# Kernel optimization log

Hardware: AMD Instinct MI355X
Metric: run time of the kernel (lower is better)

## Reference

```python
import jax, jax.numpy as jnp
import numpy as np

STACK_DEPTH = 16
SHARPEN = 5.0
LN_EPS = 1e-5
EPS = 1e-8


def _apply_tools(x, tw):
    # tools: relu, gelu(exact), tanh, sigmoid, identity; tw: [B, 5]
    return (jax.nn.relu(x) * tw[:, 0:1]
            + jax.nn.gelu(x, approximate=False) * tw[:, 1:2]
            + jnp.tanh(x) * tw[:, 2:3]
            + jax.nn.sigmoid(x) * tw[:, 3:4]
            + x * tw[:, 4:5])


def _forward(hidden_states, W_proj, b_proj, W_op, b_op, W_tool, b_tool, ln_gamma, ln_beta):
    B, S, H = hidden_states.shape
    D = STACK_DEPTH

    # Per-timestep linear ops are time-independent -> batch them up front.
    proj = jnp.einsum('bsh,ph->bsp', hidden_states, W_proj) + b_proj  # [B,S,2H]
    h_all, v_all = proj[..., :H], proj[..., H:]
    op_probs = jax.nn.softmax(jnp.einsum('bsh,oh->bso', hidden_states, W_op) + b_op, axis=-1)  # [B,S,3]
    tool_w = jax.nn.softmax(jnp.einsum('bsh,th->bst', h_all, W_tool) + b_tool, axis=-1)  # [B,S,T]

    # Differentiable stack recurrence (push/pop/nop with pointer sharpening).
    stack0 = jnp.zeros((B, D, H), hidden_states.dtype)
    pointer0 = jnp.zeros((B, D), hidden_states.dtype).at[:, 0].set(1.0)

    def step(carry, xs):
        stack, pointer = carry
        value, ops = xs  # value: [B,H], ops: [B,3]
        push, pop, nop = ops[:, 0:1], ops[:, 1:2], ops[:, 2:3]
        p_push = jnp.roll(pointer, 1, axis=1)   # pointer moves up on push
        p_pop = jnp.roll(pointer, -1, axis=1)   # pointer moves down on pop
        new_p = push * p_push + pop * p_pop + nop * pointer
        new_p = new_p ** SHARPEN
        new_p = new_p / (jnp.sum(new_p, axis=1, keepdims=True) + EPS)
        w = (push * p_push)[..., None]          # [B,D,1] write weight at pushed slot
        new_stack = stack * (1.0 - w) + value[:, None, :] * w
        top = jnp.sum(new_stack * new_p[..., None], axis=1)  # [B,H]
        return (new_stack, new_p), top

    (stack_f, pointer_f), tops = jax.lax.scan(
        step, (stack0, pointer0),
        (jnp.swapaxes(v_all, 0, 1), jnp.swapaxes(op_probs, 0, 1)))
    tops = jnp.swapaxes(tops, 0, 1)  # [B,S,H]

    processed = jax.vmap(_apply_tools, in_axes=(1, 1), out_axes=1)(tops, tool_w)  # [B,S,H]
    combined = h_all + processed + hidden_states

    mu = jnp.mean(combined, axis=-1, keepdims=True)
    var = jnp.mean((combined - mu) ** 2, axis=-1, keepdims=True)
    final = (combined - mu) * jax.lax.rsqrt(var + LN_EPS) * ln_gamma + ln_beta
    return final, stack_f, pointer_f, tool_w


def setup_inputs() -> dict:
    key = jax.random.key(0)
    ks = jax.random.split(key, 4)
    B, S, H, T = 16, 2048, 1024, 5
    sd = 1.0 / np.sqrt(H)
    return {
        'hidden_states': jax.random.normal(ks[0], (B, S, H), jnp.float32),
        'W_proj': jax.random.normal(ks[1], (2 * H, H), jnp.float32) * sd,
        'b_proj': jnp.zeros((2 * H,), jnp.float32),
        'W_op': jax.random.normal(ks[2], (3, H), jnp.float32) * sd,
        'b_op': jnp.zeros((3,), jnp.float32),
        'W_tool': jax.random.normal(ks[3], (T, H), jnp.float32) * sd,
        'b_tool': jnp.zeros((T,), jnp.float32),
        'ln_gamma': jnp.ones((H,), jnp.float32),
        'ln_beta': jnp.zeros((H,), jnp.float32),
    }


def reference(hidden_states, W_proj, b_proj, W_op, b_op, W_tool, b_tool, ln_gamma, ln_beta):
    return _forward(hidden_states, W_proj, b_proj, W_op, b_op, W_tool, b_tool, ln_gamma, ln_beta)
```

## Files before the change

kernel.cpp:

```cpp
#include <hip/hip_runtime.h>
#include <hip/hip_bf16.h>
#include <cstdint>
#include <cstdio>


typedef float f32x4 __attribute__((ext_vector_type(4)));
typedef __bf16 bf8v __attribute__((ext_vector_type(8)));

#define WS_ABF   0ULL
#define WS_WBF   67108864ULL
#define WS_PROJ  71303168ULL
#define WS_OP4   205520896ULL
#define WS_WP    206045184ULL
#define WS_NEED  210239488ULL

#define OUT_FINAL 0
#define OUT_STACK 33554432ULL
#define OUT_PTR   33816576ULL
#define OUT_TOOLW 33816832ULL
#define SLE_OFF   0ULL
#define ATOT_OFF  30000000ULL

__device__ __forceinline__ float bf2f(unsigned short u) {
    union { unsigned int i; float f; } v; v.i = ((unsigned int)u) << 16; return v.f;
}
__device__ __forceinline__ unsigned short f2bf(float f) {
    __hip_bfloat16 h = __float2bfloat16(f);
    return __builtin_bit_cast(unsigned short, h);
}
template<int C>
__device__ __forceinline__ float fdpp(float x) {
    return __int_as_float(__builtin_amdgcn_mov_dpp(__float_as_int(x), C, 0xF, 0xF, true));
}
__device__ __forceinline__ void gload_lds16(const void* g, void* l) {
    __builtin_amdgcn_global_load_lds(
        (__attribute__((address_space(1))) void*)(uintptr_t)g,
        (__attribute__((address_space(3))) void*)l,
        16, 0, 0);
}

__global__ __launch_bounds__(256) void k0(const float* __restrict__ hid,
                                          const float* __restrict__ Wp,
                                          const float* __restrict__ Wop,
                                          const float* __restrict__ bop,
                                          unsigned short* __restrict__ Abf,
                                          unsigned short* __restrict__ Wbf,
                                          float4* __restrict__ op4)
{
    const int bid = blockIdx.x, tid = threadIdx.x;
    if (bid < 8192) {
        const int wid = tid >> 6, lane = tid & 63;
        const int row = bid * 4 + wid;
        const float* hrow = hid + (size_t)row * 1024 + lane * 16;
        float xs[16];
        #pragma unroll
        for (int j = 0; j < 4; ++j) {
            float4 t = *(const float4*)(hrow + j * 4);
            xs[j*4+0] = t.x; xs[j*4+1] = t.y; xs[j*4+2] = t.z; xs[j*4+3] = t.w;
        }
        unsigned short us[16];
        #pragma unroll
        for (int j = 0; j < 16; ++j) us[j] = f2bf(xs[j]);
        uint4 ulo, uhi;
        ulo.x = (unsigned)us[0]  | ((unsigned)us[1]  << 16);
        ulo.y = (unsigned)us[2]  | ((unsigned)us[3]  << 16);
        ulo.z = (unsigned)us[4]  | ((unsigned)us[5]  << 16);
        ulo.w = (unsigned)us[6]  | ((unsigned)us[7]  << 16);
        uhi.x = (unsigned)us[8]  | ((unsigned)us[9]  << 16);
        uhi.y = (unsigned)us[10] | ((unsigned)us[11] << 16);
        uhi.z = (unsigned)us[12] | ((unsigned)us[13] << 16);
        uhi.w = (unsigned)us[14] | ((unsigned)us[15] << 16);
        unsigned short* arow = Abf + (size_t)row * 1024 + lane * 16;
        *(uint4*)(arow)     = ulo;
        *(uint4*)(arow + 8) = uhi;
        float pt[3] = {0.f, 0.f, 0.f};
        #pragma unroll
        for (int o = 0; o < 3; ++o) {
            const float* wrow = Wop + o * 1024 + lane * 16;
            #pragma unroll
            for (int j = 0; j < 4; ++j) {
                float4 t = *(const float4*)(wrow + j * 4);
                pt[o] += xs[j*4+0]*t.x + xs[j*4+1]*t.y + xs[j*4+2]*t.z + xs[j*4+3]*t.w;
            }
        }
        #pragma unroll
        for (int o = 0; o < 3; ++o)
            #pragma unroll
            for (int m = 32; m >= 1; m >>= 1) pt[o] += __shfl_xor(pt[o], m);
        if (lane == 0) {
            float l0 = pt[0] + bop[0], l1 = pt[1] + bop[1], l2 = pt[2] + bop[2];
            float mx = fmaxf(l0, fmaxf(l1, l2));
            float e0 = expf(l0 - mx), e1 = expf(l1 - mx), e2 = expf(l2 - mx);
            float inv = 1.0f / (e0 + e1 + e2);
            float4 r; r.x = e0 * inv; r.y = e1 * inv; r.z = e2 * inv; r.w = 0.f;
            op4[row] = r;
        }
    } else {
        const int b2 = bid - 8192;
        const size_t base = (size_t)b2 * 2048 + tid * 8;
        float4 a = *(const float4*)(Wp + base);
        float4 b = *(const float4*)(Wp + base + 4);
        unsigned short vs[8] = { f2bf(a.x), f2bf(a.y), f2bf(a.z), f2bf(a.w),
                                 f2bf(b.x), f2bf(b.y), f2bf(b.z), f2bf(b.w) };
        uint4 u;
        u.x = (unsigned)vs[0] | ((unsigned)vs[1] << 16);
        u.y = (unsigned)vs[2] | ((unsigned)vs[3] << 16);
        u.z = (unsigned)vs[4] | ((unsigned)vs[5] << 16);
        u.w = (unsigned)vs[6] | ((unsigned)vs[7] << 16);
        *(uint4*)(Wbf + base) = u;
    }
}

__global__ __launch_bounds__(256) void k1(const unsigned short* __restrict__ Abf,
                                          const unsigned short* __restrict__ Wbf,
                                          const float* __restrict__ bproj,
                                          unsigned short* __restrict__ proj,
                                          const float4* __restrict__ op4,
                                          float* __restrict__ wpbuf,
                                          float* __restrict__ out)
{
    __shared__ uint4 sm[2048];
    const int bid = blockIdx.x, tid = threadIdx.x;

    if (bid < 16) {
        const int b = bid;
        #pragma unroll
        for (int i = 0; i < 8; ++i)
            sm[tid + i * 256] = ((const uint4*)op4)[(size_t)b * 2048 + tid + i * 256];
        __syncthreads();
        if (tid >= 64) return;
        __builtin_amdgcn_s_setprio(1);
        const int lane = tid, d = lane & 15;
        const float probe = (float)d;
        const bool ror1_is_push = (fdpp<0x121>(probe) == (float)((d + 15) & 15));
        float p = (d == 0) ? 1.0f : 0.0f;
        float Apre = 1.0f;
        const float4* smf = (const float4*)sm;
        float4 o0 = smf[0], o1 = smf[1];
        float* wpb = wpbuf + (size_t)b * 2048 * 32;
        float* atot = out + ATOT_OFF + (size_t)b * 32 * 16;
        #pragma unroll 2
        for (int s = 0; s < 2048; ++s) {
            float4 o2 = smf[(s + 2 < 2048) ? (s + 2) : 2047];
            const float push = o0.x, pop = o0.y, nop = o0.z;
            const float ra = fdpp<0x121>(p);
            const float rb = fdpp<0x12F>(p);
            const float ppush = ror1_is_push ? ra : rb;
            const float ppop  = ror1_is_push ? rb : ra;
            const float w = push * ppush;
            float lin = push * ppush + pop * ppop + nop * p;
            float x2 = lin * lin;
            float x5 = x2 * x2 * lin;
            float sum = x5;
            sum += fdpp<0x128>(sum);
            sum += fdpp<0x124>(sum);
            sum += fdpp<0x122>(sum);
            sum += fdpp<0x121>(sum);
            float pn = x5 * __builtin_amdgcn_rcpf(sum + 1e-8f);
            const float om = 1.0f - w;
            Apre = ((s & 63) == 0) ? om : Apre * om;
            if (lane < 16) {
                float2 wp; wp.x = w; wp.y = pn;
                *(float2*)(wpb + ((size_t)s * 16 + d) * 2) = wp;
                if ((s & 63) == 63) atot[(s >> 6) * 16 + d] = Apre;
            }
            p = pn;
            o0 = o1; o1 = o2;
        }
        if (lane < 16) out[OUT_PTR + (size_t)b * 16 + d] = p;
        return;
    }

    int bid2 = bid - 16;
    bid2 = (bid2 & 7) * 512 + (bid2 >> 3);
    const int gm = bid2 & 255;
    const int gn = bid2 >> 8;
    const int wid = tid >> 6, lane = tid & 63;
    const int wm = wid & 1, wn = wid >> 1;
    const size_t row0 = (size_t)gm * 128;
    const size_t col0 = (size_t)gn * 128;
    char* smc = (char*)sm;
    const char* Ab = (const char*)Abf;
    const char* Bb = (const char*)Wbf;
    f32x4 acc[4][4];
    const f32x4 z = {0.f, 0.f, 0.f, 0.f};
    #pragma unroll
    for (int i = 0; i < 4; ++i)
        #pragma unroll
        for (int j = 0; j < 4; ++j) acc[i][j] = z;

    for (int kt = 0; kt < 16; ++kt) {
        #pragma unroll
        for (int i = 0; i < 4; ++i) {
            const int off  = (i * 256 + tid) * 16;
            const int soff = off ^ (((off >> 7) & 7) << 4);
            gload_lds16(Ab + (row0 + (size_t)(soff >> 7)) * 2048 + (size_t)kt * 128 + (soff & 127),
                        smc + (i * 256 + wid * 64) * 16);
        }
        #pragma unroll
        for (int i = 0; i < 4; ++i) {
            const int off  = (i * 256 + tid) * 16;
            const int soff = off ^ (((off >> 7) & 7) << 4);
            gload_lds16(Bb + (col0 + (size_t)(soff >> 7)) * 2048 + (size_t)kt * 128 + (soff & 127),
                        smc + 16384 + (i * 256 + wid * 64) * 16);
        }
        __syncthreads();
        bf8v af[4][2], bfv[4][2];
        #pragma unroll
        for (int mr = 0; mr < 4; ++mr)
            #pragma unroll
            for (int kk = 0; kk < 2; ++kk) {
                int byt = (wm * 64 + mr * 16 + (lane & 15)) * 128 + kk * 64 + ((lane >> 4) * 16);
                byt ^= ((byt >> 7) & 7) << 4;
                af[mr][kk] = *(const bf8v*)(smc + byt);
            }
        #pragma unroll
        for (int nr = 0; nr < 4; ++nr)
            #pragma unroll
            for (int kk = 0; kk < 2; ++kk) {
                int byt = (wn * 64 + nr * 16 + (lane & 15)) * 128 + kk * 64 + ((lane >> 4) * 16);
                byt ^= ((byt >> 7) & 7) << 4;
                bfv[nr][kk] = *(const bf8v*)(smc + 16384 + byt);
            }
        #pragma unroll
        for (int mr = 0; mr < 4; ++mr)
            #pragma unroll
            for (int nr = 0; nr < 4; ++nr) {
                acc[mr][nr] = __builtin_amdgcn_mfma_f32_16x16x32_bf16(af[mr][0], bfv[nr][0], acc[mr][nr], 0, 0, 0);
                acc[mr][nr] = __builtin_amdgcn_mfma_f32_16x16x32_bf16(af[mr][1], bfv[nr][1], acc[mr][nr], 0, 0, 0);
            }
        __syncthreads();
    }
    #pragma unroll
    for (int mr = 0; mr < 4; ++mr) {
        const int rloc = wm * 64 + mr * 16 + ((lane >> 4) * 4);
        #pragma unroll
        for (int nr = 0; nr < 4; ++nr) {
            const size_t col = col0 + wn * 64 + nr * 16 + (lane & 15);
            const float bias = bproj[col];
            #pragma unroll
            for (int j = 0; j < 4; ++j)
                proj[(row0 + rloc + j) * 2048 + col] = f2bf(acc[mr][nr][j] + bias);
        }
    }
}

__global__ __launch_bounds__(256) void k2(const unsigned short* __restrict__ proj,
                                          const float* __restrict__ wpbuf,
                                          float* __restrict__ sle)
{
    __shared__ unsigned short vlds[2][4096];
    const int bid = blockIdx.x, tid = threadIdx.x;
    const int hg = bid & 3, c = (bid >> 2) & 31, b = bid >> 7;
    if (c == 31) return;
    const int wid = tid >> 6;
    const char* vbase = (const char*)proj +
        ((size_t)(b * 2048 + c * 64) * 2048 + 1024 + hg * 256) * 2;
    const float* wpb = wpbuf + ((size_t)b * 2048 + c * 64) * 32;

    float st[16];
    #pragma unroll
    for (int d = 0; d < 16; ++d) st[d] = 0.f;

    auto STAGE = [&](int sc, int buf) {
        #pragma unroll
        for (int i = 0; i < 2; ++i) {
            const int g = i * 256 + tid;
            gload_lds16(vbase + (size_t)(sc * 16 + (g >> 5)) * 4096 + (g & 31) * 16,
                        (char*)vlds + buf * 8192 + (i * 256 + wid * 64) * 16);
        }
    };
    STAGE(0, 0);
    __syncthreads();
    for (int sc = 0; sc < 4; ++sc) {
        const int cur = sc & 1;
        if (sc < 3) STAGE(sc + 1, cur ^ 1);
        const unsigned short* vl = vlds[cur];
        #pragma unroll 4
        for (int ls = 0; ls < 16; ++ls) {
            const float v = bf2f(vl[ls * 256 + tid]);
            const float4* wp4 = (const float4*)(wpb + (size_t)(sc * 16 + ls) * 32);
            #pragma unroll
            for (int k = 0; k < 8; ++k) {
                float4 q = wp4[k];
                st[2*k]   = fmaf(q.x, v - st[2*k],   st[2*k]);
                st[2*k+1] = fmaf(q.z, v - st[2*k+1], st[2*k+1]);
            }
        }
        __syncthreads();
    }
    float* so = sle + ((size_t)b * 32 + c) * 16 * 1024 + hg * 256 + tid;
    #pragma unroll
    for (int d = 0; d < 16; ++d) so[(size_t)d * 1024] = st[d];
}

__global__ __launch_bounds__(256) void k3(const unsigned short* __restrict__ proj,
                                          const float* __restrict__ wpbuf,
                                          const float* __restrict__ sle,
                                          const float* __restrict__ atot,
                                          unsigned short* __restrict__ tops,
                                          float* __restrict__ out)
{
    __shared__ unsigned short vlds[2][4096];
    const int bid = blockIdx.x, tid = threadIdx.x;
    const int hg = bid & 3, c = (bid >> 2) & 31, b = bid >> 7;
    const int wid = tid >> 6;
    const char* vbase = (const char*)proj +
        ((size_t)(b * 2048 + c * 64) * 2048 + 1024 + hg * 256) * 2;
    const float* wpb = wpbuf + ((size_t)b * 2048 + c * 64) * 32;

    float st[16];
    #pragma unroll
    for (int d = 0; d < 16; ++d) st[d] = 0.f;

    {
        const float* sb = sle + (size_t)b * 32 * 16 * 1024 + hg * 256 + tid;
        const float* ab = atot + (size_t)b * 32 * 16;
        for (int cp = 0; cp < c; ++cp) {
            #pragma unroll
            for (int d = 0; d < 16; ++d)
                st[d] = fmaf(ab[cp * 16 + d], st[d],
                             sb[((size_t)cp * 16 + d) * 1024]);
        }
    }

    unsigned short* topb = tops + ((size_t)b * 2048 + c * 64) * 1024 + hg * 256 + tid;

    auto STAGE = [&](int sc, int buf) {
        #pragma unroll
        for (int i = 0; i < 2; ++i) {
            const int g = i * 256 + tid;
            gload_lds16(vbase + (size_t)(sc * 16 + (g >> 5)) * 4096 + (g & 31) * 16,
                        (char*)vlds + buf * 8192 + (i * 256 + wid * 64) * 16);
        }
    };
    STAGE(0, 0);
    __syncthreads();
    for (int sc = 0; sc < 4; ++sc) {
        const int cur = sc & 1;
        if (sc < 3) STAGE(sc + 1, cur ^ 1);
        const unsigned short* vl = vlds[cur];
        #pragma unroll 4
        for (int ls = 0; ls < 16; ++ls) {
            const float v = bf2f(vl[ls * 256 + tid]);
            const float4* wp4 = (const float4*)(wpb + (size_t)(sc * 16 + ls) * 32);
            float t0 = 0.f, t1 = 0.f;
            #pragma unroll
            for (int k = 0; k < 8; ++k) {
                float4 q = wp4[k];
                st[2*k]   = fmaf(q.x, v - st[2*k],   st[2*k]);
                st[2*k+1] = fmaf(q.z, v - st[2*k+1], st[2*k+1]);
                t0 = fmaf(q.y, st[2*k],   t0);
                t1 = fmaf(q.w, st[2*k+1], t1);
            }
            topb[(size_t)(sc * 16 + ls) * 1024] = f2bf(t0 + t1);
        }
        __syncthreads();
    }
    if (c == 31) {
        #pragma unroll
        for (int d = 0; d < 16; ++d)
            out[OUT_STACK + ((size_t)b * 16 + d) * 1024 + hg * 256 + tid] = st[d];
    }
}

__global__ __launch_bounds__(256) void k5(const unsigned short* __restrict__ proj,
                                          const unsigned short* __restrict__ tops,
                                          const float* __restrict__ hid,
                                          const float* __restrict__ Wtool,
                                          const float* __restrict__ btool,
                                          const float* __restrict__ gamma,
                                          const float* __restrict__ beta,
                                          float* __restrict__ out)
{
    __shared__ float red[4][8];
    const int row = blockIdx.x, tid = threadIdx.x;
    const int wid = tid >> 6, lane = tid & 63;
    const int k0i = tid * 4;
    uint2 hu = *(const uint2*)(proj + (size_t)row * 2048 + k0i);
    float hh[4];
    hh[0] = bf2f(hu.x & 0xffff); hh[1] = bf2f(hu.x >> 16);
    hh[2] = bf2f(hu.y & 0xffff); hh[3] = bf2f(hu.y >> 16);
    uint2 tu = *(const uint2*)(tops + (size_t)row * 1024 + k0i);
    float xs[4];
    xs[0] = bf2f(tu.x & 0xffff); xs[1] = bf2f(tu.x >> 16);
    xs[2] = bf2f(tu.y & 0xffff); xs[3] = bf2f(tu.y >> 16);
    float4 hd4 = *(const float4*)(hid + (size_t)row * 1024 + k0i);
    float hds[4] = {hd4.x, hd4.y, hd4.z, hd4.w};
    float pt[5];
    #pragma unroll
    for (int t = 0; t < 5; ++t) {
        float4 wv = *(const float4*)(Wtool + t * 1024 + k0i);
        pt[t] = hh[0]*wv.x + hh[1]*wv.y + hh[2]*wv.z + hh[3]*wv.w;
    }
    #pragma unroll
    for (int t = 0; t < 5; ++t)
        #pragma unroll
        for (int m = 32; m >= 1; m >>= 1) pt[t] += __shfl_xor(pt[t], m);
    if (lane == 0) {
        #pragma unroll
        for (int t = 0; t < 5; ++t) red[wid][t] = pt[t];
    }
    __syncthreads();
    float tw[5];
    {
        float lg[5];
        #pragma unroll
        for (int t = 0; t < 5; ++t)
            lg[t] = red[0][t] + red[1][t] + red[2][t] + red[3][t] + btool[t];
        float mx = fmaxf(fmaxf(fmaxf(lg[0], lg[1]), fmaxf(lg[2], lg[3])), lg[4]);
        float se = 0.f;
        #pragma unroll
        for (int t = 0; t < 5; ++t) { tw[t] = expf(lg[t] - mx); se += tw[t]; }
        float inv = 1.0f / se;
        #pragma unroll
        for (int t = 0; t < 5; ++t) tw[t] *= inv;
    }
    if (tid < 5) out[OUT_TOOLW + (size_t)row * 5 + tid] = tw[tid];
    float cj[4];
    #pragma unroll
    for (int j = 0; j < 4; ++j) {
        const float x = xs[j];
        const float rl = fmaxf(x, 0.f);
        const float gl = 0.5f * x * (1.f + erff(x * 0.70710678118654752f));
        const float th = tanhf(x);
        const float sg = 1.f / (1.f + expf(-x));
        const float pr = rl*tw[0] + gl*tw[1] + th*tw[2] + sg*tw[3] + x*tw[4];
        cj[j] = hh[j] + pr + hds[j];
    }
    float s1 = cj[0] + cj[1] + cj[2] + cj[3];
    float s2 = cj[0]*cj[0] + cj[1]*cj[1] + cj[2]*cj[2] + cj[3]*cj[3];
    #pragma unroll
    for (int m = 32; m >= 1; m >>= 1) { s1 += __shfl_xor(s1, m); s2 += __shfl_xor(s2, m); }
    __syncthreads();
    if (lane == 0) { red[wid][0] = s1; red[wid][1] = s2; }
    __syncthreads();
    const float S1 = red[0][0] + red[1][0] + red[2][0] + red[3][0];
    const float S2 = red[0][1] + red[1][1] + red[2][1] + red[3][1];
    const float mu = S1 * (1.f / 1024.f);
    const float var = S2 * (1.f / 1024.f) - mu * mu;
    const float rstd = rsqrtf(var + 1e-5f);
    float4 g4 = *(const float4*)(gamma + k0i);
    float4 b4 = *(const float4*)(beta + k0i);
    float4 res;
    res.x = (cj[0] - mu) * rstd * g4.x + b4.x;
    res.y = (cj[1] - mu) * rstd * g4.y + b4.y;
    res.z = (cj[2] - mu) * rstd * g4.z + b4.z;
    res.w = (cj[3] - mu) * rstd * g4.w + b4.w;
    *(float4*)(out + (size_t)row * 1024 + k0i) = res;
}

extern "C" void kernel_launch(void* const* d_in, const int* in_sizes, int n_in,
                              void* d_out, int out_size, void* d_ws, size_t ws_size,
                              hipStream_t stream)
{
    if (ws_size < WS_NEED) {
        fprintf(stderr, "kernel_launch: ws_size %zu < required %llu\n",
                ws_size, (unsigned long long)WS_NEED);
        return;
    }
    const float* hid = (const float*)d_in[0];
    const float* Wp  = (const float*)d_in[1];
    const float* bp  = (const float*)d_in[2];
    const float* Wop = (const float*)d_in[3];
    const float* bop = (const float*)d_in[4];
    const float* Wtl = (const float*)d_in[5];
    const float* btl = (const float*)d_in[6];
    const float* gam = (const float*)d_in[7];
    const float* bet = (const float*)d_in[8];
    float* out = (float*)d_out;
    char* ws = (char*)d_ws;
    unsigned short* Abf  = (unsigned short*)(ws + WS_ABF);
    unsigned short* Wbf  = (unsigned short*)(ws + WS_WBF);
    unsigned short* proj = (unsigned short*)(ws + WS_PROJ);
    float4* op4 = (float4*)(ws + WS_OP4);
    float* wpbuf = (float*)(ws + WS_WP);
    float* sle  = out + SLE_OFF;
    float* atot = out + ATOT_OFF;

    k0<<<9216, 256, 0, stream>>>(hid, Wp, Wop, bop, Abf, Wbf, op4);
    k1<<<4112, 256, 0, stream>>>(Abf, Wbf, bp, proj, op4, wpbuf, out);
    k2<<<2048, 256, 0, stream>>>(proj, wpbuf, sle);
    k3<<<2048, 256, 0, stream>>>(proj, wpbuf, sle, atot, Abf, out);
    k5<<<32768, 256, 0, stream>>>(proj, Abf, hid, Wtl, btl, gam, bet, out);
}
```

Measured before the change: 554.3 us.

## Double-buffer GEMM LDS tiles, remap XCD tiles, add chunk-prefix scan kernel

The projection GEMM now double-buffers its A/B tiles in LDS, issuing the next k-tile's loads before computing the current one, so global loads overlap MFMA work. Block-to-tile mapping is changed so each XCD handles a contiguous set of row tiles across all column tiles, which is meant to improve L2 reuse of A. The O(c) serial prefix over chunk summaries in k3 is replaced by a separate k2b kernel that computes each chunk's starting stack state once. k3 then just loads 16 values per thread, at the cost of an extra launch and extra global traffic, and the GEMM uses double the LDS.

```diff
diff --git a/kernel.cpp b/kernel.cpp
--- a/kernel.cpp
+++ b/kernel.cpp
@@ -18,8 +18,9 @@
 #define OUT_STACK 33554432ULL
 #define OUT_PTR   33816576ULL
 #define OUT_TOOLW 33816832ULL
-#define SLE_OFF   0ULL
-#define ATOT_OFF  30000000ULL
+#define SLE_OFF    0ULL
+#define SSTART_OFF 9437184ULL
+#define ATOT_OFF   30000000ULL
 
 __device__ __forceinline__ float bf2f(unsigned short u) {
     union { unsigned int i; float f; } v; v.i = ((unsigned int)u) << 16; return v.f;
@@ -119,7 +120,7 @@
                                           float* __restrict__ wpbuf,
                                           float* __restrict__ out)
 {
-    __shared__ uint4 sm[2048];
+    __shared__ uint4 sm[4096];
     const int bid = blockIdx.x, tid = threadIdx.x;
 
     if (bid < 16) {
@@ -171,10 +172,10 @@
         return;
     }
 
-    int bid2 = bid - 16;
-    bid2 = (bid2 & 7) * 512 + (bid2 >> 3);
-    const int gm = bid2 & 255;
-    const int gn = bid2 >> 8;
+    const int li = bid - 16;
+    const int xcd = li & 7, j = li >> 3;
+    const int gm = xcd * 32 + (j >> 4);
+    const int gn = j & 15;
     const int wid = tid >> 6, lane = tid & 63;
     const int wm = wid & 1, wn = wid >> 1;
     const size_t row0 = (size_t)gm * 128;
@@ -187,24 +188,32 @@
     #pragma unroll
     for (int i = 0; i < 4; ++i)
         #pragma unroll
-        for (int j = 0; j < 4; ++j) acc[i][j] = z;
-
-    for (int kt = 0; kt < 16; ++kt) {
+        for (int jj = 0; jj < 4; ++jj) acc[i][jj] = z;
+
+    auto STAGE = [&](int kt, int buf) {
         #pragma unroll
         for (int i = 0; i < 4; ++i) {
             const int off  = (i * 256 + tid) * 16;
             const int soff = off ^ (((off >> 7) & 7) << 4);
             gload_lds16(Ab + (row0 + (size_t)(soff >> 7)) * 2048 + (size_t)kt * 128 + (soff & 127),
-                        smc + (i * 256 + wid * 64) * 16);
+                        smc + buf * 32768 + (i * 256 + wid * 64) * 16);
         }
         #pragma unroll
         for (int i = 0; i < 4; ++i) {
             const int off  = (i * 256 + tid) * 16;
             const int soff = off ^ (((off >> 7) & 7) << 4);
             gload_lds16(Bb + (col0 + (size_t)(soff >> 7)) * 2048 + (size_t)kt * 128 + (soff & 127),
-                        smc + 16384 + (i * 256 + wid * 64) * 16);
-        }
-        __syncthreads();
+                        smc + buf * 32768 + 16384 + (i * 256 + wid * 64) * 16);
+        }
+    };
+
+    STAGE(0, 0);
+    __syncthreads();
+    for (int kt = 0; kt < 16; ++kt) {
+        const int cur = kt & 1;
+        if (kt < 15) STAGE(kt + 1, cur ^ 1);
+        const char* ab = smc + cur * 32768;
+        const char* bb = ab + 16384;
         bf8v af[4][2], bfv[4][2];
         #pragma unroll
         for (int mr = 0; mr < 4; ++mr)
@@ -212,7 +221,7 @@
             for (int kk = 0; kk < 2; ++kk) {
                 int byt = (wm * 64 + mr * 16 + (lane & 15)) * 128 + kk * 64 + ((lane >> 4) * 16);
                 byt ^= ((byt >> 7) & 7) << 4;
-                af[mr][kk] = *(const bf8v*)(smc + byt);
+                af[mr][kk] = *(const bf8v*)(ab + byt);
             }
         #pragma unroll
         for (int nr = 0; nr < 4; ++nr)
@@ -220,7 +229,7 @@
             for (int kk = 0; kk < 2; ++kk) {
                 int byt = (wn * 64 + nr * 16 + (lane & 15)) * 128 + kk * 64 + ((lane >> 4) * 16);
                 byt ^= ((byt >> 7) & 7) << 4;
-                bfv[nr][kk] = *(const bf8v*)(smc + 16384 + byt);
+                bfv[nr][kk] = *(const bf8v*)(bb + byt);
             }
         #pragma unroll
         for (int mr = 0; mr < 4; ++mr)
@@ -239,8 +248,8 @@
             const size_t col = col0 + wn * 64 + nr * 16 + (lane & 15);
             const float bias = bproj[col];
             #pragma unroll
-            for (int j = 0; j < 4; ++j)
-                proj[(row0 + rloc + j) * 2048 + col] = f2bf(acc[mr][nr][j] + bias);
+            for (int jj = 0; jj < 4; ++jj)
+                proj[(row0 + rloc + jj) * 2048 + col] = f2bf(acc[mr][nr][jj] + bias);
         }
     }
 }
@@ -294,10 +303,28 @@
     for (int d = 0; d < 16; ++d) so[(size_t)d * 1024] = st[d];
 }
 
+__global__ __launch_bounds__(256) void k2b(const float* __restrict__ sle,
+                                           const float* __restrict__ atot,
+                                           float* __restrict__ sstart)
+{
+    const int bid = blockIdx.x, tid = threadIdx.x;
+    const int hg = bid & 3, d = (bid >> 2) & 15, b = bid >> 6;
+    const int h = hg * 256 + tid;
+    const float* sb = sle    + ((size_t)b * 512 + d) * 1024 + h;
+    float*       so = sstart + ((size_t)b * 512 + d) * 1024 + h;
+    const float* ab = atot + (size_t)b * 512 + d;
+    float st = 0.f;
+    #pragma unroll 4
+    for (int c = 0; c < 31; ++c) {
+        so[(size_t)c * 16384] = st;
+        st = fmaf(ab[c * 16], st, sb[(size_t)c * 16384]);
+    }
+    so[31ull * 16384] = st;
+}
+
 __global__ __launch_bounds__(256) void k3(const unsigned short* __restrict__ proj,
                                           const float* __restrict__ wpbuf,
-                                          const float* __restrict__ sle,
-                                          const float* __restrict__ atot,
+                                          const float* __restrict__ sstart,
                                           unsigned short* __restrict__ tops,
                                           float* __restrict__ out)
 {
@@ -310,18 +337,10 @@
     const float* wpb = wpbuf + ((size_t)b * 2048 + c * 64) * 32;
 
     float st[16];
-    #pragma unroll
-    for (int d = 0; d < 16; ++d) st[d] = 0.f;
-
     {
-        const float* sb = sle + (size_t)b * 32 * 16 * 1024 + hg * 256 + tid;
-        const float* ab = atot + (size_t)b * 32 * 16;
-        for (int cp = 0; cp < c; ++cp) {
-            #pragma unroll
-            for (int d = 0; d < 16; ++d)
-                st[d] = fmaf(ab[cp * 16 + d], st[d],
-                             sb[((size_t)cp * 16 + d) * 1024]);
-        }
+        const float* ss = sstart + ((size_t)b * 32 + c) * 16 * 1024 + hg * 256 + tid;
+        #pragma unroll
+        for (int d = 0; d < 16; ++d) st[d] = ss[(size_t)d * 1024];
     }
 
     unsigned short* topb = tops + ((size_t)b * 2048 + c * 64) * 1024 + hg * 256 + tid;
@@ -475,12 +494,14 @@
     unsigned short* proj = (unsigned short*)(ws + WS_PROJ);
     float4* op4 = (float4*)(ws + WS_OP4);
     float* wpbuf = (float*)(ws + WS_WP);
-    float* sle  = out + SLE_OFF;
-    float* atot = out + ATOT_OFF;
+    float* sle    = out + SLE_OFF;
+    float* sstart = out + SSTART_OFF;
+    float* atot   = out + ATOT_OFF;
 
     k0<<<9216, 256, 0, stream>>>(hid, Wp, Wop, bop, Abf, Wbf, op4);
     k1<<<4112, 256, 0, stream>>>(Abf, Wbf, bp, proj, op4, wpbuf, out);
     k2<<<2048, 256, 0, stream>>>(proj, wpbuf, sle);
-    k3<<<2048, 256, 0, stream>>>(proj, wpbuf, sle, atot, Abf, out);
+    k2b<<<1024, 256, 0, stream>>>(sle, atot, sstart);
+    k3<<<2048, 256, 0, stream>>>(proj, wpbuf, sstart, Abf, out);
     k5<<<32768, 256, 0, stream>>>(proj, Abf, hid, Wtl, btl, gam, bet, out);
 }
```

Measured after the change: 576.1 us. 3.9% more time.
